# Kernel tuning notes

Measured on AMD Instinct MI355X. Metric: run time of the kernel, lower is better.

The kernel has to match this reference:

```python
import jax, jax.numpy as jnp
import numpy as np

B, D, H, W, C = 4, 8, 16, 16, 512
K_RED = 8
R = C // K_RED          # reduced channels for Q/K
EPS = 1e-3              # keras LayerNormalization default epsilon


def setup_inputs() -> dict:
    key = jax.random.key(0)
    ks = jax.random.split(key, 8)
    s = 0.02
    f32 = jnp.float32
    return {
        "x":  jax.random.normal(ks[0], (B, D, H, W, C), f32),
        # 1x1x1 Conv3D == per-position linear over channels
        "wq": (jax.random.normal(ks[1], (C, R), f32) * s), "bq": jnp.zeros((R,), f32),
        "wk": (jax.random.normal(ks[2], (C, R), f32) * s), "bk": jnp.zeros((R,), f32),
        "wv": (jax.random.normal(ks[3], (C, C), f32) * s), "bv": jnp.zeros((C,), f32),
        "wm": (jax.random.normal(ks[4], (C, C), f32) * s), "bm": jnp.zeros((C,), f32),
        "g1": jnp.ones((C,), f32), "b1": jnp.zeros((C,), f32),
        "g2": jnp.ones((C,), f32), "b2": jnp.zeros((C,), f32),
    }


def _layer_norm(x, g, b):
    m = jnp.mean(x, axis=-1, keepdims=True)
    v = jnp.mean(jnp.square(x - m), axis=-1, keepdims=True)
    return (x - m) * jax.lax.rsqrt(v + EPS) * g + b


def reference(x, wq, bq, wk, bk, wv, bv, wm, bm, g1, b1, g2, b2):
    b, d, h, w, c = x.shape
    f = h * w
    xf = x.reshape(b, d, f, c)                      # [B,D,F,C]
    Q = xf @ wq + bq                                # [B,D,F,R]
    K = xf @ wk + bk                                # [B,D,F,R]
    V = xf @ wv + bv                                # [B,D,F,C]
    # full global scores: [B, D, F, D, F]
    e = jnp.einsum('bifr,bgjr->bifgj', Q, K)
    alphas = jax.nn.softmax(e.reshape(b, d, f, d * f), axis=-1)
    alphas = alphas.reshape(b, d, f, d, f)
    # original einsum 'bdfgh,bdhi->bdfi' sums over key-depth g and uses V at
    # the query depth d; fold the g-sum first, then per-depth F x F matmul.
    a2 = alphas.sum(axis=3)                         # [B,D,F,F]
    attn = jnp.einsum('bdfh,bdhc->bdfc', a2, V)     # [B,D,F,C]
    y1 = _layer_norm(attn + xf, g1, b1)
    y2 = _layer_norm(y1 + jax.nn.relu(y1 @ wm + bm), g2, b2)
    return y2.reshape(b, d, h, w, c)
```

## Files before the change

### kernel.cpp

```cpp
#include <hip/hip_runtime.h>
#include <cstdint>

#define LN_EPS 1e-3f
using u16 = unsigned short;
using u32 = unsigned int;
typedef __attribute__((ext_vector_type(8))) short bh8;
typedef __attribute__((ext_vector_type(4))) float f4;
#define MFMA16(A,B,C) __builtin_amdgcn_mfma_f32_16x16x32_bf16((A),(B),(C),0,0,0)
#define SBAR() __builtin_amdgcn_s_barrier()
#define CFENCE() asm volatile("" ::: "memory")
#define WAITV(N) asm volatile("s_waitcnt vmcnt(" #N ")" ::: "memory")

__device__ __forceinline__ u16 bf16r(float f){
    union{float f;u32 u;} c; c.f=f;
    return (u16)((c.u + 0x7fffu + ((c.u>>16)&1u))>>16);
}
__device__ __forceinline__ u32 pk2(float a, float b){
    return (u32)bf16r(a) | ((u32)bf16r(b)<<16);
}
__device__ __forceinline__ void glds16(const void* g, void* l){
    __builtin_amdgcn_global_load_lds(
        (const __attribute__((address_space(1))) u32*)g,
        (__attribute__((address_space(3))) u32*)l, 16, 0, 0);
}

__global__ __launch_bounds__(256) void k0_prep(
    const float* __restrict__ wq, const float* __restrict__ wk,
    const float* __restrict__ wv, const float* __restrict__ wm,
    u16* __restrict__ wqkv_p, u16* __restrict__ wm_p)
{
    const int t = threadIdx.x;
    const int c = t & 15, qn = t >> 4;
    const int quad = qn & 3, ntl = qn >> 2;
    const int blk = blockIdx.x;
    if (blk < 32){
        const int s = blk >> 1, hh = blk & 1;
        const int krow = s*32 + quad*8;
        u16* dst = wqkv_p + (size_t)s*20480;
        #pragma unroll
        for (int i=0;i<5;++i){
            const int nt = hh*20 + i*4 + ntl;
            const int n = nt*16 + c;
            const float* src; int ldw;
            if (n < 64){ src = wq + (size_t)krow*64 + n; ldw = 64; }
            else if (n < 128){ src = wk + (size_t)krow*64 + (n-64); ldw = 64; }
            else { src = wv + (size_t)krow*512 + (n-128); ldw = 512; }
            float v[8];
            #pragma unroll
            for (int j=0;j<8;++j) v[j] = src[(size_t)j*ldw];
            uint4 o; o.x=pk2(v[0],v[1]); o.y=pk2(v[2],v[3]); o.z=pk2(v[4],v[5]); o.w=pk2(v[6],v[7]);
            *(uint4*)&dst[((nt*4+quad)*16 + c)*8] = o;
        }
    } else {
        const int bb = blk - 32;
        const int s = bb >> 1, hh = bb & 1;
        const int krow = s*32 + quad*8;
        u16* dst = wm_p + (size_t)s*16384;
        #pragma unroll
        for (int i=0;i<4;++i){
            const int nt = hh*16 + i*4 + ntl;
            const int n = nt*16 + c;
            const float* src = wm + (size_t)krow*512 + n;
            float v[8];
            #pragma unroll
            for (int j=0;j<8;++j) v[j] = src[(size_t)j*512];
            uint4 o; o.x=pk2(v[0],v[1]); o.y=pk2(v[2],v[3]); o.z=pk2(v[4],v[5]); o.w=pk2(v[6],v[7]);
            *(uint4*)&dst[((nt*4+quad)*16 + c)*8] = o;
        }
    }
}

__global__ __launch_bounds__(512) void k1_qkv(
    const float* __restrict__ x, const float* __restrict__ bq, const float* __restrict__ bk,
    const u16* __restrict__ wqkv_p,
    u16* __restrict__ Qb, u16* __restrict__ Kb, u16* __restrict__ Vb)
{
    __shared__ u16 Asf[16384];
    __shared__ u16 Bs[2][20480];
    const int t = threadIdx.x, w = t>>6, lane = t&63, quad = (lane>>4)&3, c = lane&15;
    const int rg = w>>2, cg = w&3;
    const int rowbase = blockIdx.x << 5;

    #pragma unroll
    for (int i=0;i<5;++i)
        glds16((const char*)wqkv_p + (size_t)w*5120 + i*1024 + lane*16,
               (char*)Bs[0] + w*5120 + i*1024);
    #pragma unroll
    for (int i=0;i<8;++i){
        const int idx = t + (i<<9);
        const int fr = idx >> 7, fc4 = idx & 127;
        float4 xv = *(const float4*)&x[(size_t)(rowbase+fr)*512 + fc4*4];
        uint2 pkv; pkv.x = pk2(xv.x,xv.y); pkv.y = pk2(xv.z,xv.w);
        const int s = fc4 >> 3, qd = (fc4 >> 1) & 3, j0 = (fc4 & 1)*4;
        *(uint2*)&Asf[(fr>>4)*8192 + s*512 + (qd*16 + (fr&15))*8 + j0] = pkv;
    }
    f4 acc[10];
    #pragma unroll
    for (int i=0;i<10;++i) acc[i] = (f4){0.f,0.f,0.f,0.f};
    __syncthreads();

    for (int s=0;s<16;++s){
        const u16* Bcur = Bs[s&1];
        bh8 a = *(const bh8*)&Asf[rg*8192 + s*512 + (quad*16+c)*8];
        if (s+1 < 16){
            #pragma unroll
            for (int i=0;i<5;++i)
                glds16((const char*)wqkv_p + (size_t)(s+1)*40960 + (size_t)w*5120 + i*1024 + lane*16,
                       (char*)Bs[(s+1)&1] + w*5120 + i*1024);
            WAITV(5);
        } else {
            WAITV(0);
        }
        SBAR(); CFENCE();
        __builtin_amdgcn_s_setprio(1);
        #pragma unroll
        for (int nt2=0;nt2<10;++nt2){
            bh8 bb = *(const bh8*)&Bcur[((cg*10+nt2)*4 + quad)*128 + c*8];
            acc[nt2] = MFMA16(a, bb, acc[nt2]);
        }
        __builtin_amdgcn_s_setprio(0);
        CFENCE(); SBAR();
    }

    const int rt = (blockIdx.x<<1) + rg;
    const int bd = rowbase >> 8;
    const int kloc = (rowbase & 255) + rg*16 + quad*4;
    const int sv = kloc >> 5, kq = (kloc >> 3) & 3, jk0 = kloc & 7;
    #pragma unroll
    for (int nt2=0;nt2<10;++nt2){
        const int colb = cg*160 + nt2*16;
        if (colb < 128){
            const bool isK = (colb >= 64);
            const int r = colb - (isK ? 64 : 0) + c;
            const float bias = isK ? bk[r] : bq[r];
            u16* dstb = (isK ? Kb : Qb) + ((size_t)(rt*2 + (r>>5))*4 + ((r>>3)&3))*128 + (r&7);
            #pragma unroll
            for (int reg=0;reg<4;++reg)
                dstb[(quad*4+reg)*8] = bf16r(acc[nt2][reg] + bias);
        } else {
            const int ntv = (colb - 128) >> 4;
            u16* dstv = Vb + (size_t)bd*131072 + (size_t)sv*16384
                           + (size_t)((ntv*4+kq)*128 + c*8 + jk0);
            ushort4 o;
            o.x = bf16r(acc[nt2][0]); o.y = bf16r(acc[nt2][1]);
            o.z = bf16r(acc[nt2][2]); o.w = bf16r(acc[nt2][3]);
            *(ushort4*)dstv = o;
        }
    }
}

__global__ __launch_bounds__(512) void k234(
    const u16* __restrict__ Qb, const u16* __restrict__ Kb, const u16* __restrict__ Vb,
    const u16* __restrict__ wm_p,
    const float* __restrict__ x, const float* __restrict__ bv,
    const float* __restrict__ g1, const float* __restrict__ b1,
    const float* __restrict__ bm, const float* __restrict__ g2, const float* __restrict__ b2,
    float* __restrict__ out)
{
    __shared__ u16 Bs[2][16384];
    __shared__ u16 y1f[16384];
    __shared__ u16 a2f[8192];
    __shared__ u16 qsf[2048];
    __shared__ float redA[2][4][16], redB[2][4][16];
    const int t = threadIdx.x, w = t>>6, lane = t&63, quad = (lane>>4)&3, c = lane&15;
    const int rg = w>>2, cg = w&3;
    const int bd = blockIdx.x & 31, ftile = blockIdx.x >> 5;
    const int b = bd >> 3;
    const int rowbase = (bd<<8) + (ftile<<5);
    const int rt00 = rowbase >> 4;
    const char* Kbase = (const char*)Kb + (size_t)b*262144;
    const char* Vbase = (const char*)Vb + (size_t)bd*262144;

    if (w < 4) glds16((const char*)Qb + (size_t)rt00*2048 + w*1024 + lane*16,
                      (char*)qsf + w*1024);
    #pragma unroll
    for (int i=0;i<4;++i)
        glds16(Kbase + (size_t)w*4096 + i*1024 + lane*16, (char*)Bs[0] + w*4096 + i*1024);
    __syncthreads();
    bh8 aq0 = *(const bh8*)&qsf[rg*1024 + (quad*16+c)*8];
    bh8 aq1 = *(const bh8*)&qsf[rg*1024 + 512 + (quad*16+c)*8];

    float lp[4] = {0.f,0.f,0.f,0.f};
    float a2r[4][4] = {};
    for (int cc=0; cc<8; ++cc){
        const u16* Bcur = Bs[cc&1];
        if (cc+1 < 8){
            #pragma unroll
            for (int i=0;i<4;++i)
                glds16(Kbase + (size_t)(cc+1)*32768 + (size_t)w*4096 + i*1024 + lane*16,
                       (char*)Bs[(cc+1)&1] + w*4096 + i*1024);
            WAITV(4);
        } else {
            WAITV(0);
        }
        SBAR(); CFENCE();
        __builtin_amdgcn_s_setprio(1);
        f4 sa[4];
        #pragma unroll
        for (int kt=0;kt<4;++kt){
            sa[kt] = (f4){0.f,0.f,0.f,0.f};
            bh8 b0 = *(const bh8*)&Bcur[(cg*4+kt)*1024 + (quad*16+c)*8];
            bh8 bv1= *(const bh8*)&Bcur[(cg*4+kt)*1024 + 512 + (quad*16+c)*8];
            sa[kt] = MFMA16(aq0, b0, sa[kt]);
            sa[kt] = MFMA16(aq1, bv1, sa[kt]);
        }
        __builtin_amdgcn_s_setprio(0);
        #pragma unroll
        for (int kt=0;kt<4;++kt)
            #pragma unroll
            for (int reg=0;reg<4;++reg){
                float e = __expf(sa[kt][reg]);
                lp[reg] += e;
                a2r[reg][kt] += e;
            }
        CFENCE(); SBAR();
    }
    #pragma unroll
    for (int i=0;i<4;++i)
        glds16(Vbase + (size_t)w*4096 + i*1024 + lane*16, (char*)Bs[0] + w*4096 + i*1024);
    #pragma unroll
    for (int reg=0;reg<4;++reg){
        float v = lp[reg];
        v += __shfl_xor(v,1,64); v += __shfl_xor(v,2,64);
        v += __shfl_xor(v,4,64); v += __shfl_xor(v,8,64);
        lp[reg] = v;
    }
    if (c==0){
        #pragma unroll
        for (int reg=0;reg<4;++reg) redA[rg][cg][quad*4+reg] = lp[reg];
    }
    __syncthreads();
    float fac[4];
    #pragma unroll
    for (int reg=0;reg<4;++reg){
        const int q = quad*4+reg;
        fac[reg] = 1.f/(redA[rg][0][q]+redA[rg][1][q]+redA[rg][2][q]+redA[rg][3][q]);
    }
    #pragma unroll
    for (int reg=0;reg<4;++reg)
        #pragma unroll
        for (int kt=0;kt<4;++kt){
            const int jp = cg*64 + kt*16 + c;
            a2f[rg*4096 + (jp>>5)*512 + (((jp>>3)&3)*16 + quad*4+reg)*8 + (jp&7)]
                = bf16r(a2r[reg][kt]*fac[reg]);
        }
    __syncthreads();

    f4 cacc[8];
    #pragma unroll
    for (int i=0;i<8;++i) cacc[i] = (f4){0.f,0.f,0.f,0.f};
    for (int s8=0;s8<8;++s8){
        const u16* Bcur = Bs[s8&1];
        bh8 a = *(const bh8*)&a2f[rg*4096 + s8*512 + (quad*16+c)*8];
        if (s8+1 < 8){
            #pragma unroll
            for (int i=0;i<4;++i)
                glds16(Vbase + (size_t)(s8+1)*32768 + (size_t)w*4096 + i*1024 + lane*16,
                       (char*)Bs[(s8+1)&1] + w*4096 + i*1024);
            WAITV(4);
        } else {
            WAITV(0);
        }
        SBAR(); CFENCE();
        __builtin_amdgcn_s_setprio(1);
        #pragma unroll
        for (int nt2=0;nt2<8;++nt2){
            bh8 bb = *(const bh8*)&Bcur[((cg*8+nt2)*4 + quad)*128 + c*8];
            cacc[nt2] = MFMA16(a, bb, cacc[nt2]);
        }
        __builtin_amdgcn_s_setprio(0);
        CFENCE(); SBAR();
    }

    {
        float sv4[4] = {0.f,0.f,0.f,0.f}, qv2[4] = {0.f,0.f,0.f,0.f};
        #pragma unroll
        for (int nt2=0;nt2<8;++nt2){
            const int col = cg*128 + nt2*16 + c;
            const float bvv = bv[col];
            #pragma unroll
            for (int reg=0;reg<4;++reg){
                const int row = rowbase + rg*16 + quad*4 + reg;
                float val = cacc[nt2][reg] + bvv + x[(size_t)row*512 + col];
                cacc[nt2][reg] = val;
                sv4[reg] += val; qv2[reg] = fmaf(val,val,qv2[reg]);
            }
        }
        #pragma unroll
        for (int reg=0;reg<4;++reg){
            float s1=sv4[reg], s2=qv2[reg];
            s1 += __shfl_xor(s1,1,64); s2 += __shfl_xor(s2,1,64);
            s1 += __shfl_xor(s1,2,64); s2 += __shfl_xor(s2,2,64);
            s1 += __shfl_xor(s1,4,64); s2 += __shfl_xor(s2,4,64);
            s1 += __shfl_xor(s1,8,64); s2 += __shfl_xor(s2,8,64);
            sv4[reg]=s1; qv2[reg]=s2;
        }
        if (c==0){
            #pragma unroll
            for (int reg=0;reg<4;++reg){ redA[rg][cg][quad*4+reg]=sv4[reg]; redB[rg][cg][quad*4+reg]=qv2[reg]; }
        }
        __syncthreads();
        float mean[4], rstd[4];
        #pragma unroll
        for (int reg=0;reg<4;++reg){
            const int q = quad*4+reg;
            const float S  = redA[rg][0][q]+redA[rg][1][q]+redA[rg][2][q]+redA[rg][3][q];
            const float Q2 = redB[rg][0][q]+redB[rg][1][q]+redB[rg][2][q]+redB[rg][3][q];
            const float m = S*(1.f/512.f);
            mean[reg]=m; rstd[reg]=rsqrtf(Q2*(1.f/512.f) - m*m + LN_EPS);
        }
        #pragma unroll
        for (int nt2=0;nt2<8;++nt2){
            const int col = cg*128 + nt2*16 + c;
            const float gg = g1[col], bb1 = b1[col];
            #pragma unroll
            for (int reg=0;reg<4;++reg){
                float y = (cacc[nt2][reg]-mean[reg])*rstd[reg]*gg + bb1;
                cacc[nt2][reg] = y;
                y1f[rg*8192 + (col>>5)*512 + (((col>>3)&3)*16 + quad*4+reg)*8 + (col&7)] = bf16r(y);
            }
        }
        #pragma unroll
        for (int i=0;i<4;++i)
            glds16((const char*)wm_p + (size_t)w*4096 + i*1024 + lane*16,
                   (char*)Bs[0] + w*4096 + i*1024);
        __syncthreads();
    }

    f4 dacc[8];
    #pragma unroll
    for (int i=0;i<8;++i) dacc[i] = (f4){0.f,0.f,0.f,0.f};
    for (int s=0;s<16;++s){
        const u16* Bcur = Bs[s&1];
        bh8 a = *(const bh8*)&y1f[rg*8192 + s*512 + (quad*16+c)*8];
        if (s+1 < 16){
            #pragma unroll
            for (int i=0;i<4;++i)
                glds16((const char*)wm_p + (size_t)(s+1)*32768 + (size_t)w*4096 + i*1024 + lane*16,
                       (char*)Bs[(s+1)&1] + w*4096 + i*1024);
            WAITV(4);
        } else {
            WAITV(0);
        }
        SBAR(); CFENCE();
        __builtin_amdgcn_s_setprio(1);
        #pragma unroll
        for (int nt2=0;nt2<8;++nt2){
            bh8 bb = *(const bh8*)&Bcur[((cg*8+nt2)*4 + quad)*128 + c*8];
            dacc[nt2] = MFMA16(a, bb, dacc[nt2]);
        }
        __builtin_amdgcn_s_setprio(0);
        CFENCE(); SBAR();
    }

    {
        float sv4[4] = {0.f,0.f,0.f,0.f}, qv2[4] = {0.f,0.f,0.f,0.f};
        #pragma unroll
        for (int nt2=0;nt2<8;++nt2){
            const int col = cg*128 + nt2*16 + c;
            const float bmv = bm[col];
            #pragma unroll
            for (int reg=0;reg<4;++reg){
                float hh = fmaxf(dacc[nt2][reg]+bmv, 0.f) + cacc[nt2][reg];
                dacc[nt2][reg] = hh;
                sv4[reg] += hh; qv2[reg] = fmaf(hh,hh,qv2[reg]);
            }
        }
        #pragma unroll
        for (int reg=0;reg<4;++reg){
            float s1=sv4[reg], s2=qv2[reg];
            s1 += __shfl_xor(s1,1,64); s2 += __shfl_xor(s2,1,64);
            s1 += __shfl_xor(s1,2,64); s2 += __shfl_xor(s2,2,64);
            s1 += __shfl_xor(s1,4,64); s2 += __shfl_xor(s2,4,64);
            s1 += __shfl_xor(s1,8,64); s2 += __shfl_xor(s2,8,64);
            sv4[reg]=s1; qv2[reg]=s2;
        }
        if (c==0){
            #pragma unroll
            for (int reg=0;reg<4;++reg){ redA[rg][cg][quad*4+reg]=sv4[reg]; redB[rg][cg][quad*4+reg]=qv2[reg]; }
        }
        __syncthreads();
        float mean[4], rstd[4];
        #pragma unroll
        for (int reg=0;reg<4;++reg){
            const int q = quad*4+reg;
            const float S  = redA[rg][0][q]+redA[rg][1][q]+redA[rg][2][q]+redA[rg][3][q];
            const float Q2 = redB[rg][0][q]+redB[rg][1][q]+redB[rg][2][q]+redB[rg][3][q];
            const float m = S*(1.f/512.f);
            mean[reg]=m; rstd[reg]=rsqrtf(Q2*(1.f/512.f) - m*m + LN_EPS);
        }
        #pragma unroll
        for (int nt2=0;nt2<8;++nt2){
            const int col = cg*128 + nt2*16 + c;
            const float gg = g2[col], bb2 = b2[col];
            #pragma unroll
            for (int reg=0;reg<4;++reg){
                const int row = rowbase + rg*16 + quad*4 + reg;
                out[(size_t)row*512 + col] = (dacc[nt2][reg]-mean[reg])*rstd[reg]*gg + bb2;
            }
        }
    }
}

extern "C" void kernel_launch(void* const* d_in, const int* in_sizes, int n_in,
                              void* d_out, int out_size, void* d_ws, size_t ws_size,
                              hipStream_t stream) {
    (void)in_sizes; (void)n_in; (void)out_size; (void)ws_size;
    const float* x  = (const float*)d_in[0];
    const float* wq = (const float*)d_in[1];
    const float* bq = (const float*)d_in[2];
    const float* wk = (const float*)d_in[3];
    const float* bk = (const float*)d_in[4];
    const float* wv = (const float*)d_in[5];
    const float* bv = (const float*)d_in[6];
    const float* wm = (const float*)d_in[7];
    const float* bm = (const float*)d_in[8];
    const float* g1 = (const float*)d_in[9];
    const float* b1 = (const float*)d_in[10];
    const float* g2 = (const float*)d_in[11];
    const float* b2 = (const float*)d_in[12];

    u16* wqkv_p = (u16*)d_ws;
    u16* wm_p   = wqkv_p + 327680;
    u16* Qb     = wm_p   + 262144;
    u16* Kb     = Qb     + 524288;
    u16* Vb     = Kb     + 524288;
    float* outp = (float*)d_out;

    k0_prep<<<64, 256, 0, stream>>>(wq, wk, wv, wm, wqkv_p, wm_p);
    k1_qkv <<<256, 512, 0, stream>>>(x, bq, bk, wqkv_p, Qb, Kb, Vb);
    k234   <<<256, 512, 0, stream>>>(Qb, Kb, Vb, wm_p, x, bv, g1, b1, bm, g2, b2, outp);
}
```

Measured before the change: 143.9 us.

## Triple-buffer weight and K/V tiles with two-stage lookahead prefetch

After: 140.2 us. 1.03x faster.

```diff
diff --git a/kernel.cpp b/kernel.cpp
--- a/kernel.cpp
+++ b/kernel.cpp
@@ -10,6 +10,8 @@
 #define SBAR() __builtin_amdgcn_s_barrier()
 #define CFENCE() asm volatile("" ::: "memory")
 #define WAITV(N) asm volatile("s_waitcnt vmcnt(" #N ")" ::: "memory")
+#define LKBAR() do{ asm volatile("s_waitcnt lgkmcnt(0)" ::: "memory"); \
+                    __builtin_amdgcn_s_barrier(); asm volatile("" ::: "memory"); }while(0)
 
 __device__ __forceinline__ u16 bf16r(float f){
     union{float f;u32 u;} c; c.f=f;
@@ -76,7 +78,7 @@
     u16* __restrict__ Qb, u16* __restrict__ Kb, u16* __restrict__ Vb)
 {
     __shared__ u16 Asf[16384];
-    __shared__ u16 Bs[2][20480];
+    __shared__ u16 Bs[3][20480];
     const int t = threadIdx.x, w = t>>6, lane = t&63, quad = (lane>>4)&3, c = lane&15;
     const int rg = w>>2, cg = w&3;
     const int rowbase = blockIdx.x << 5;
@@ -85,6 +87,10 @@
     for (int i=0;i<5;++i)
         glds16((const char*)wqkv_p + (size_t)w*5120 + i*1024 + lane*16,
                (char*)Bs[0] + w*5120 + i*1024);
+    #pragma unroll
+    for (int i=0;i<5;++i)
+        glds16((const char*)wqkv_p + 40960 + (size_t)w*5120 + i*1024 + lane*16,
+               (char*)Bs[1] + w*5120 + i*1024);
     #pragma unroll
     for (int i=0;i<8;++i){
         const int idx = t + (i<<9);
@@ -97,16 +103,19 @@
     f4 acc[10];
     #pragma unroll
     for (int i=0;i<10;++i) acc[i] = (f4){0.f,0.f,0.f,0.f};
-    __syncthreads();
-
+    LKBAR();
+
+    #pragma unroll
     for (int s=0;s<16;++s){
-        const u16* Bcur = Bs[s&1];
+        const u16* Bcur = Bs[s%3];
         bh8 a = *(const bh8*)&Asf[rg*8192 + s*512 + (quad*16+c)*8];
-        if (s+1 < 16){
+        if (s+2 < 16){
             #pragma unroll
             for (int i=0;i<5;++i)
-                glds16((const char*)wqkv_p + (size_t)(s+1)*40960 + (size_t)w*5120 + i*1024 + lane*16,
-                       (char*)Bs[(s+1)&1] + w*5120 + i*1024);
+                glds16((const char*)wqkv_p + (size_t)(s+2)*40960 + (size_t)w*5120 + i*1024 + lane*16,
+                       (char*)Bs[(s+2)%3] + w*5120 + i*1024);
+            WAITV(10);
+        } else if (s+1 < 16){
             WAITV(5);
         } else {
             WAITV(0);
@@ -157,7 +166,7 @@
     const float* __restrict__ bm, const float* __restrict__ g2, const float* __restrict__ b2,
     float* __restrict__ out)
 {
-    __shared__ u16 Bs[2][16384];
+    __shared__ u16 Bs[3][16384];
     __shared__ u16 y1f[16384];
     __shared__ u16 a2f[8192];
     __shared__ u16 qsf[2048];
@@ -176,19 +185,26 @@
     #pragma unroll
     for (int i=0;i<4;++i)
         glds16(Kbase + (size_t)w*4096 + i*1024 + lane*16, (char*)Bs[0] + w*4096 + i*1024);
-    __syncthreads();
+    #pragma unroll
+    for (int i=0;i<4;++i)
+        glds16(Kbase + 32768 + (size_t)w*4096 + i*1024 + lane*16, (char*)Bs[1] + w*4096 + i*1024);
+    WAITV(8);
+    SBAR(); CFENCE();
     bh8 aq0 = *(const bh8*)&qsf[rg*1024 + (quad*16+c)*8];
     bh8 aq1 = *(const bh8*)&qsf[rg*1024 + 512 + (quad*16+c)*8];
 
     float lp[4] = {0.f,0.f,0.f,0.f};
     float a2r[4][4] = {};
+    #pragma unroll
     for (int cc=0; cc<8; ++cc){
-        const u16* Bcur = Bs[cc&1];
-        if (cc+1 < 8){
+        const u16* Bcur = Bs[cc%3];
+        if (cc+2 < 8){
             #pragma unroll
             for (int i=0;i<4;++i)
-                glds16(Kbase + (size_t)(cc+1)*32768 + (size_t)w*4096 + i*1024 + lane*16,
-                       (char*)Bs[(cc+1)&1] + w*4096 + i*1024);
+                glds16(Kbase + (size_t)(cc+2)*32768 + (size_t)w*4096 + i*1024 + lane*16,
+                       (char*)Bs[(cc+2)%3] + w*4096 + i*1024);
+            WAITV(8);
+        } else if (cc+1 < 8){
             WAITV(4);
         } else {
             WAITV(0);
@@ -219,6 +235,9 @@
     for (int i=0;i<4;++i)
         glds16(Vbase + (size_t)w*4096 + i*1024 + lane*16, (char*)Bs[0] + w*4096 + i*1024);
     #pragma unroll
+    for (int i=0;i<4;++i)
+        glds16(Vbase + 32768 + (size_t)w*4096 + i*1024 + lane*16, (char*)Bs[1] + w*4096 + i*1024);
+    #pragma unroll
     for (int reg=0;reg<4;++reg){
         float v = lp[reg];
         v += __shfl_xor(v,1,64); v += __shfl_xor(v,2,64);
@@ -229,7 +248,7 @@
         #pragma unroll
         for (int reg=0;reg<4;++reg) redA[rg][cg][quad*4+reg] = lp[reg];
     }
-    __syncthreads();
+    LKBAR();
     float fac[4];
     #pragma unroll
     for (int reg=0;reg<4;++reg){
@@ -244,19 +263,22 @@
             a2f[rg*4096 + (jp>>5)*512 + (((jp>>3)&3)*16 + quad*4+reg)*8 + (jp&7)]
                 = bf16r(a2r[reg][kt]*fac[reg]);
         }
-    __syncthreads();
+    LKBAR();
 
     f4 cacc[8];
     #pragma unroll
     for (int i=0;i<8;++i) cacc[i] = (f4){0.f,0.f,0.f,0.f};
+    #pragma unroll
     for (int s8=0;s8<8;++s8){
-        const u16* Bcur = Bs[s8&1];
+        const u16* Bcur = Bs[s8%3];
         bh8 a = *(const bh8*)&a2f[rg*4096 + s8*512 + (quad*16+c)*8];
-        if (s8+1 < 8){
+        if (s8+2 < 8){
             #pragma unroll
             for (int i=0;i<4;++i)
-                glds16(Vbase + (size_t)(s8+1)*32768 + (size_t)w*4096 + i*1024 + lane*16,
-                       (char*)Bs[(s8+1)&1] + w*4096 + i*1024);
+                glds16(Vbase + (size_t)(s8+2)*32768 + (size_t)w*4096 + i*1024 + lane*16,
+                       (char*)Bs[(s8+2)%3] + w*4096 + i*1024);
+            WAITV(8);
+        } else if (s8+1 < 8){
             WAITV(4);
         } else {
             WAITV(0);
@@ -271,6 +293,15 @@
         __builtin_amdgcn_s_setprio(0);
         CFENCE(); SBAR();
     }
+
+    #pragma unroll
+    for (int i=0;i<4;++i)
+        glds16((const char*)wm_p + (size_t)w*4096 + i*1024 + lane*16,
+               (char*)Bs[0] + w*4096 + i*1024);
+    #pragma unroll
+    for (int i=0;i<4;++i)
+        glds16((const char*)wm_p + 32768 + (size_t)w*4096 + i*1024 + lane*16,
+               (char*)Bs[1] + w*4096 + i*1024);
 
     {
         float sv4[4] = {0.f,0.f,0.f,0.f}, qv2[4] = {0.f,0.f,0.f,0.f};
@@ -299,7 +330,7 @@
             #pragma unroll
             for (int reg=0;reg<4;++reg){ redA[rg][cg][quad*4+reg]=sv4[reg]; redB[rg][cg][quad*4+reg]=qv2[reg]; }
         }
-        __syncthreads();
+        LKBAR();
         float mean[4], rstd[4];
         #pragma unroll
         for (int reg=0;reg<4;++reg){
@@ -320,24 +351,23 @@
                 y1f[rg*8192 + (col>>5)*512 + (((col>>3)&3)*16 + quad*4+reg)*8 + (col&7)] = bf16r(y);
             }
         }
-        #pragma unroll
-        for (int i=0;i<4;++i)
-            glds16((const char*)wm_p + (size_t)w*4096 + i*1024 + lane*16,
-                   (char*)Bs[0] + w*4096 + i*1024);
-        __syncthreads();
+        LKBAR();
     }
 
     f4 dacc[8];
     #pragma unroll
     for (int i=0;i<8;++i) dacc[i] = (f4){0.f,0.f,0.f,0.f};
+    #pragma unroll
     for (int s=0;s<16;++s){
-        const u16* Bcur = Bs[s&1];
+        const u16* Bcur = Bs[s%3];
         bh8 a = *(const bh8*)&y1f[rg*8192 + s*512 + (quad*16+c)*8];
-        if (s+1 < 16){
+        if (s+2 < 16){
             #pragma unroll
             for (int i=0;i<4;++i)
-                glds16((const char*)wm_p + (size_t)(s+1)*32768 + (size_t)w*4096 + i*1024 + lane*16,
-                       (char*)Bs[(s+1)&1] + w*4096 + i*1024);
+                glds16((const char*)wm_p + (size_t)(s+2)*32768 + (size_t)w*4096 + i*1024 + lane*16,
+                       (char*)Bs[(s+2)%3] + w*4096 + i*1024);
+            WAITV(8);
+        } else if (s+1 < 16){
             WAITV(4);
         } else {
             WAITV(0);
```
